# Kernel tuning notes

Measured on AMD Instinct MI355X. Metric: run time of the kernel, lower is better.

Reference implementation:

```python
import jax, jax.numpy as jnp
from jax import lax
import numpy as np

NLAYERS = 3
NHID = 256
NINP = 128
K = 2          # nstride (conv kernel size)
B = 32
W = 512


def _lstm_conv_layer(x_list, hid, ctx, conv_ws, conv_bs, rw, rb, aw):
    """One LSTM_conv(nl=len(conv_ws)) forward.
    x_list: list of [B, H, W]; hid: [nl+1, B, H, K]; ctx: [nl, B, H, K].
    Returns hx_all [B,H,W], cx_all [B,H,W], attn [B,W-1].
    """
    nl = len(conv_ws)
    ig = None
    for j in range(nl):
        # left-pad with last K-1 hidden columns, 'VALID' conv of kernel K -> length W
        padded = jnp.concatenate([hid[j][:, :, 1:], x_list[j]], axis=2)  # [B,H,W+K-1]
        y = lax.conv_general_dilated(padded, conv_ws[j], (1,), 'VALID',
                                     dimension_numbers=('NCH', 'OIH', 'NCH'))
        y = y + conv_bs[j][None, :, None]
        ig = y if ig is None else ig + y          # [B, 4H, W]

    hx0 = hid[nl][:, :, K - 1]                    # [B, H]
    cx0 = ctx[nl - 1][:, :, K - 1]                # [B, H]
    wsz = ig.shape[-1]
    ig_t = jnp.transpose(ig, (2, 0, 1))           # [W, B, 4H]
    not_last = jnp.arange(wsz) < (wsz - 1)

    def step(carry, inp):
        hx, cx = carry
        g_t, nl_flag = inp
        gates = g_t + hx @ rw.T + rb              # [B, 4H]
        i_g, f_g, c_g, o_g = jnp.split(gates, 4, axis=-1)  # torch fused LSTM order
        cx = jax.nn.sigmoid(f_g) * cx + jax.nn.sigmoid(i_g) * jnp.tanh(c_g)
        hx = jax.nn.sigmoid(o_g) * jnp.tanh(cx)
        a = jax.nn.sigmoid(hx @ aw)               # [B]
        hx = jnp.where(nl_flag, hx * a[:, None], hx)  # gate applied except at last step
        return (hx, cx), (hx, cx, a)

    _, (hs, cs, a_s) = lax.scan(step, (hx0, cx0), (ig_t, not_last))
    hx_all = jnp.transpose(hs, (1, 2, 0))         # [B, H, W]
    cx_all = jnp.transpose(cs, (1, 2, 0))
    attn = a_s[:-1].T                             # [B, W-1]
    return hx_all, cx_all, attn


def setup_inputs() -> dict:
    key = jax.random.key(0)
    ks = jax.random.split(key, 10)
    s = 0.02
    return {
        'input':   jax.random.normal(ks[0], (B, NINP, W), jnp.float32),
        'hidden':  jax.random.normal(ks[1], (NLAYERS + 1, B, NHID, K), jnp.float32),
        'context': jax.random.normal(ks[2], (NLAYERS, B, NHID, K), jnp.float32),
        'emb_w':   jax.random.normal(ks[3], (NHID, NINP), jnp.float32) * s,
        'emb_b':   jax.random.normal(ks[4], (NHID,), jnp.float32) * s,
        'conv_w':  jax.random.normal(ks[5], (6, 4 * NHID, NHID, K), jnp.float32) * s,
        'conv_b':  jax.random.normal(ks[6], (6, 4 * NHID), jnp.float32) * s,
        'rec_w':   jax.random.normal(ks[7], (NLAYERS, 4 * NHID, NHID), jnp.float32) * s,
        'rec_b':   jax.random.normal(ks[8], (NLAYERS, 4 * NHID), jnp.float32) * s,
        'attn_w':  jax.random.normal(ks[9], (NLAYERS, NHID), jnp.float32) * s,
    }


def reference(input, hidden, context, emb_w, emb_b, conv_w, conv_b, rec_w, rec_b, attn_w):
    # emb: Conv1d(ninp, nhid, 1)
    x0 = jnp.einsum('oc,bcw->bow', emb_w, input) + emb_b[None, :, None]  # [B,H,W]
    x_list = [x0]
    next_ctx = []
    attns = []
    off = 0
    for l in range(NLAYERS):
        nl = l + 1
        hx_all, cx_all, attn = _lstm_conv_layer(
            x_list, hidden[:nl + 1], context[:nl],
            [conv_w[off + j] for j in range(nl)],
            [conv_b[off + j] for j in range(nl)],
            rec_w[l], rec_b[l], attn_w[l])
        off += nl
        x_list.append(hx_all)
        next_ctx.append(cx_all)
        attns.append(attn)
    x = jnp.stack(x_list, 0)                      # [NLAYERS+1, B, H, W]
    nc = jnp.stack(next_ctx, 0)                   # [NLAYERS, B, H, W]
    attns = jnp.stack(attns, 0)                   # [NLAYERS, B, W-1]
    return x[:, :, :, -K:], nc[:, :, :, -K:], attns
```

## Files before the change

kernel.cpp:

```cpp
#include <hip/hip_runtime.h>


typedef _Float16 h2 __attribute__((ext_vector_type(2)));

static __device__ __forceinline__ float fdot2(unsigned a, unsigned b, float c) {
#if __has_builtin(__builtin_amdgcn_fdot2)
  return __builtin_amdgcn_fdot2(__builtin_bit_cast(h2, a),
                                __builtin_bit_cast(h2, b), c, false);
#else
  h2 x = __builtin_bit_cast(h2, a), y = __builtin_bit_cast(h2, b);
  return c + (float)x[0] * (float)y[0] + (float)x[1] * (float)y[1];
#endif
}

static __device__ __forceinline__ unsigned short f16b(float v) {
  _Float16 h = (_Float16)v;
  return __builtin_bit_cast(unsigned short, h);
}

static __device__ __forceinline__ float sigm(float x) {
  return 1.0f / (1.0f + __expf(-x));
}
static __device__ __forceinline__ float tanh_(float x) {
  return 1.0f - 2.0f / (1.0f + __expf(2.0f * x));
}

__global__ __launch_bounds__(256) void prep_rw(const float* __restrict__ rw,
                                               unsigned* __restrict__ rwp) {
  int idx = blockIdx.x * 256 + threadIdx.x;
  if (idx >= 3 * 131072) return;
  int l = idx / 131072, pos = idx % 131072;
  int tid, rl, j;
  if (pos < 98304) {
    int d = pos >> 9;
    tid = pos & 511;
    rl = d / 24;
    j = d % 24;
  } else {
    int p = pos - 98304;
    int c = p >> 11, rem = p & 2047;
    tid = rem >> 2;
    int k = rem & 3;
    rl = c >> 1;
    j = 24 + (c & 1) * 4 + k;
  }
  int s = tid & 3, u = tid >> 2;
  int row = (rl >> 1) * 256 + (rl & 1) * 128 + u;
  int cp = s * 32 + j;
  const float* src = rw + (l * 1024 + row) * 256 + 2 * cp;
  rwp[idx] = (unsigned)f16b(src[0]) | ((unsigned)f16b(src[1]) << 16);
}

__global__ __launch_bounds__(256) void prep_cw(const float* __restrict__ cw,
                                               unsigned* __restrict__ cwp) {
  int idx = blockIdx.x * 256 + threadIdx.x;
  if (idx >= 6 * 1024 * 2 * 128) return;
  int d = idx & 127, k = (idx >> 7) & 1, o = (idx >> 8) & 1023, jj = idx >> 18;
  const float* src = cw + ((jj * 1024 + o) * 256 + 2 * d) * 2 + k;
  unsigned v = (unsigned)f16b(src[0]) | ((unsigned)f16b(src[2]) << 16);
  cwp[idx] = v;
}

__global__ __launch_bounds__(256) void emb_kernel(
    const float* __restrict__ inp, const float* __restrict__ ew,
    const float* __restrict__ eb, unsigned short* __restrict__ x0f,
    float* __restrict__ out) {
  __shared__ float xt[32][65];
  __shared__ float wt[64][33];
  int b = blockIdx.z, w0 = blockIdx.x * 64, h0 = blockIdx.y * 64;
  int tid = threadIdx.x, tx = tid & 15, ty = tid >> 4;
  float acc[4][4] = {};
  for (int c0 = 0; c0 < 128; c0 += 32) {
    __syncthreads();
#pragma unroll
    for (int i = 0; i < 8; i++) {
      int f = i * 256 + tid, c = f >> 6, wl = f & 63;
      xt[c][wl] = inp[(b * 128 + c0 + c) * 512 + w0 + wl];
    }
#pragma unroll
    for (int i = 0; i < 8; i++) {
      int f = i * 256 + tid, h = f >> 5, c = f & 31;
      wt[h][c] = ew[(h0 + h) * 128 + c0 + c];
    }
    __syncthreads();
#pragma unroll
    for (int c = 0; c < 32; c++) {
      float xv[4], wv[4];
#pragma unroll
      for (int q = 0; q < 4; q++) xv[q] = xt[c][ty * 4 + q];
#pragma unroll
      for (int p = 0; p < 4; p++) wv[p] = wt[tx * 4 + p][c];
#pragma unroll
      for (int q = 0; q < 4; q++)
#pragma unroll
        for (int p = 0; p < 4; p++) acc[q][p] += xv[q] * wv[p];
    }
  }
#pragma unroll
  for (int q = 0; q < 4; q++) {
    int w = w0 + ty * 4 + q;
#pragma unroll
    for (int p = 0; p < 4; p++) {
      int h = h0 + tx * 4 + p;
      float v = acc[q][p] + eb[h];
      x0f[(b * 512 + w) * 256 + h] = f16b(v);
      if (w >= 510) out[(b * 256 + h) * 2 + (w - 510)] = v;
    }
  }
}

__global__ __launch_bounds__(256) void conv_kernel(
    const unsigned short* __restrict__ xf, const unsigned* __restrict__ cwp,
    const float* __restrict__ cb, const float* __restrict__ hidden,
    unsigned short* __restrict__ igf, int l, int off) {
  __shared__ __align__(16) unsigned xs[65][20];
  __shared__ __align__(16) unsigned wsm[2][16][66];
  int b = blockIdx.z, w0 = blockIdx.x * 64, o0 = blockIdx.y * 64;
  int tid = threadIdx.x, tx = tid & 15, ty = tid >> 4;
  float acc[4][4] = {};
  int nl = l + 1;
  for (int j = 0; j < nl; j++) {
    const unsigned* xj = (const unsigned*)(xf + j * 4194304 + b * 512 * 256);
    const unsigned* cwj = cwp + (off + j) * 262144;
    for (int c0 = 0; c0 < 256; c0 += 32) {
      int d0 = c0 >> 1;
      __syncthreads();
#pragma unroll
      for (int i = 0; i < 5; i++) {
        int f = i * 256 + tid;
        if (f < 1040) {
          int col = f >> 4, dw = f & 15;
          int w = w0 - 1 + col;
          unsigned v;
          if (w >= 0) {
            v = xj[w * 128 + d0 + dw];
          } else {
            const float* hp = hidden + ((j * 32 + b) * 256 + 2 * (d0 + dw)) * 2 + 1;
            v = (unsigned)f16b(hp[0]) | ((unsigned)f16b(hp[2]) << 16);
          }
          xs[col][dw] = v;
        }
      }
#pragma unroll
      for (int i = 0; i < 8; i++) {
        int f = i * 256 + tid;
        int oo = f >> 5, k = (f >> 4) & 1, dw = f & 15;
        wsm[k][dw][oo] = cwj[(o0 + oo) * 256 + k * 128 + d0 + dw];
      }
      __syncthreads();
#pragma unroll
      for (int g = 0; g < 4; g++) {
        uint4 xv[5];
#pragma unroll
        for (int q = 0; q < 5; q++)
          xv[q] = *(const uint4*)&xs[ty * 4 + q][g * 4];
#pragma unroll
        for (int p = 0; p < 4; p++) {
          unsigned wv0[4], wv1[4];
#pragma unroll
          for (int r = 0; r < 4; r++) {
            wv0[r] = wsm[0][g * 4 + r][tx * 4 + p];
            wv1[r] = wsm[1][g * 4 + r][tx * 4 + p];
          }
#pragma unroll
          for (int q = 0; q < 4; q++) {
            float a = acc[q][p];
            a = fdot2(wv0[0], xv[q].x, a);
            a = fdot2(wv0[1], xv[q].y, a);
            a = fdot2(wv0[2], xv[q].z, a);
            a = fdot2(wv0[3], xv[q].w, a);
            a = fdot2(wv1[0], xv[q + 1].x, a);
            a = fdot2(wv1[1], xv[q + 1].y, a);
            a = fdot2(wv1[2], xv[q + 1].z, a);
            a = fdot2(wv1[3], xv[q + 1].w, a);
            acc[q][p] = a;
          }
        }
      }
    }
  }
#pragma unroll
  for (int p = 0; p < 4; p++) {
    int o = o0 + tx * 4 + p;
    float bias = 0.f;
    for (int j = 0; j < nl; j++) bias += cb[(off + j) * 1024 + o];
#pragma unroll
    for (int q = 0; q < 4; q++) {
      int w = w0 + ty * 4 + q;
      igf[(b * 512 + w) * 1024 + o] = f16b(acc[q][p] + bias);
    }
  }
}

__global__ __launch_bounds__(512)
__attribute__((amdgpu_waves_per_eu(2, 2)))
void rec_kernel(const _Float16* __restrict__ igf, const unsigned* __restrict__ rwp_l,
                const float* __restrict__ rb, const float* __restrict__ aw,
                const float* __restrict__ hidden, const float* __restrict__ context,
                int l, unsigned short* __restrict__ xnext, float* __restrict__ out) {
  __shared__ __align__(16) uint4 w_lds4[16 * 512];
  __shared__ __align__(16) unsigned short hx_buf[2][256];
  __shared__ float red[2][8];
  int b = blockIdx.x, tid = threadIdx.x;
  int s = tid & 3, u = tid >> 2, lane = tid & 63, wid = tid >> 6;
  int hh = s & 1;
  int u2 = u + 128 * hh;

  unsigned wv[192];
#pragma unroll
  for (int d = 0; d < 192; d++) wv[d] = rwp_l[d * 512 + tid];
#pragma unroll
  for (int d = 0; d < 192; d++) asm volatile("" : "+v"(wv[d]));

  {
    const uint4* g16 = (const uint4*)(rwp_l + 98304);
#pragma unroll
    for (int c = 0; c < 16; c++) w_lds4[c * 512 + tid] = g16[c * 512 + tid];
  }

  float rb0 = rb[u2], rb1 = rb[256 + u2], rb2 = rb[512 + u2], rb3 = rb[768 + u2];
  float awj = aw[u2];
  float cx = context[((l * 32 + b) * 256 + u2) * 2 + 1];
  if (tid < 256)
    hx_buf[1][tid] = f16b(hidden[(((l + 1) * 32 + b) * 256 + tid) * 2 + 1]);
  float h_prev = 0.f;
  __syncthreads();

  const _Float16* igb = igf + (b * 512) * 1024 + u2;

  for (int t = 0; t < 512; t++) {
    int cur = t & 1, prv = cur ^ 1;
    const _Float16* ip = igb + t * 1024;
    float ig0 = (float)ip[0], ig1 = (float)ip[256];
    float ig2 = (float)ip[512], ig3 = (float)ip[768];
    float m_ = 1.0f;
    if (t) {
      const float* rp = red[prv];
      m_ = sigm(((rp[0] + rp[1]) + (rp[2] + rp[3])) +
                ((rp[4] + rp[5]) + (rp[6] + rp[7])));
    }

    float acc[8] = {};
    const uint4* hq = ((const uint4*)hx_buf[prv]) + 8 * s;
#pragma unroll
    for (int q = 0; q < 6; q++) {
      uint4 h = hq[q];
#pragma unroll
      for (int rl = 0; rl < 8; rl++) {
        acc[rl] = fdot2(wv[rl * 24 + q * 4 + 0], h.x, acc[rl]);
        acc[rl] = fdot2(wv[rl * 24 + q * 4 + 1], h.y, acc[rl]);
        acc[rl] = fdot2(wv[rl * 24 + q * 4 + 2], h.z, acc[rl]);
        acc[rl] = fdot2(wv[rl * 24 + q * 4 + 3], h.w, acc[rl]);
      }
    }
#pragma unroll
    for (int q = 6; q < 8; q++) {
      uint4 h = hq[q];
#pragma unroll
      for (int rl = 0; rl < 8; rl++) {
        uint4 lw = w_lds4[(rl * 2 + (q - 6)) * 512 + tid];
        acc[rl] = fdot2(lw.x, h.x, acc[rl]);
        acc[rl] = fdot2(lw.y, h.y, acc[rl]);
        acc[rl] = fdot2(lw.z, h.z, acc[rl]);
        acc[rl] = fdot2(lw.w, h.w, acc[rl]);
      }
    }
#pragma unroll
    for (int rl = 0; rl < 8; rl++) acc[rl] += __shfl_xor(acc[rl], 1);
#pragma unroll
    for (int rl = 0; rl < 8; rl++) acc[rl] += __shfl_xor(acc[rl], 2);

    float di = hh ? acc[1] : acc[0];
    float df = hh ? acc[3] : acc[2];
    float dc = hh ? acc[5] : acc[4];
    float do_ = hh ? acc[7] : acc[6];
    float g_i = ig0 + rb0 + m_ * di;
    float g_f = ig1 + rb1 + m_ * df;
    float g_c = ig2 + rb2 + m_ * dc;
    float g_o = ig3 + rb3 + m_ * do_;
    cx = sigm(g_f) * cx + sigm(g_i) * tanh_(g_c);
    float h_raw = sigm(g_o) * tanh_(cx);

    float part = (s < 2) ? h_raw * awj : 0.f;
#pragma unroll
    for (int sh = 32; sh > 0; sh >>= 1) part += __shfl_xor(part, sh);
    if (lane == 0) red[cur][wid] = part;

    if (s < 2) {
      hx_buf[cur][u2] = f16b(h_raw);
      if (t) {
        float hg = h_prev * m_;
        xnext[(b * 512 + (t - 1)) * 256 + u2] = f16b(hg);
        if (t == 511)
          out[(((l + 1) * 32 + b) * 256 + u2) * 2 + 0] = hg;
      }
      if (t >= 510)
        out[65536 + ((l * 32 + b) * 256 + u2) * 2 + (t - 510)] = cx;
    }
    if (tid == 0 && t) out[114688 + (l * 32 + b) * 511 + (t - 1)] = m_;
    h_prev = h_raw;
    __syncthreads();
  }
  if (s < 2) {
    xnext[(b * 512 + 511) * 256 + u2] = f16b(h_prev);
    out[(((l + 1) * 32 + b) * 256 + u2) * 2 + 1] = h_prev;
  }
}

extern "C" void kernel_launch(void* const* d_in, const int* in_sizes, int n_in,
                              void* d_out, int out_size, void* d_ws,
                              size_t ws_size, hipStream_t stream) {
  const float* input  = (const float*)d_in[0];
  const float* hidden = (const float*)d_in[1];
  const float* context= (const float*)d_in[2];
  const float* emb_w  = (const float*)d_in[3];
  const float* emb_b  = (const float*)d_in[4];
  const float* conv_w = (const float*)d_in[5];
  const float* conv_b = (const float*)d_in[6];
  const float* rec_w  = (const float*)d_in[7];
  const float* rec_b  = (const float*)d_in[8];
  const float* attn_w = (const float*)d_in[9];
  float* out = (float*)d_out;

  char* ws = (char*)d_ws;
  unsigned short* xf16 = (unsigned short*)ws;
  _Float16* igf = (_Float16*)(ws + 33554432);
  unsigned* rwp = (unsigned*)(ws + 67108864);
  unsigned* cwp = (unsigned*)(ws + 68681728);

  hipLaunchKernelGGL(prep_rw, dim3(1536), dim3(256), 0, stream, rec_w, rwp);
  hipLaunchKernelGGL(prep_cw, dim3(6144), dim3(256), 0, stream, conv_w, cwp);
  hipLaunchKernelGGL(emb_kernel, dim3(8, 4, 32), dim3(256), 0, stream,
                     input, emb_w, emb_b, xf16, out);
  int off = 0;
  for (int l = 0; l < 3; l++) {
    hipLaunchKernelGGL(conv_kernel, dim3(8, 16, 32), dim3(256), 0, stream,
                       xf16, cwp, conv_b, hidden, (unsigned short*)igf, l, off);
    hipLaunchKernelGGL(rec_kernel, dim3(32), dim3(512), 0, stream,
                       igf, rwp + l * 131072, rec_b + l * 1024,
                       attn_w + l * 256, hidden, context, l,
                       xf16 + (l + 1) * 4194304, out);
    off += l + 1;
  }
}
```

Measured before the change: 4.427 ms.

## Process two batch rows per recurrent block to reuse register-resident weights

The recurrent kernel now handles two batch elements per block (16 blocks instead of 32). Each weight fetched from registers or LDS is applied to both hidden vectors, and the threads that previously idled in the gate phase (s>=2) now compute the second batch's gates. To make room for the doubled accumulators, fewer weight words stay in registers (184 instead of 192) and more go to LDS, with the prep layout changed to match. The cost is twice the FMA work per block on each serial timestep, and only half the CUs are occupied.

```diff
diff --git a/kernel.cpp b/kernel.cpp
--- a/kernel.cpp
+++ b/kernel.cpp
@@ -31,18 +31,30 @@
   if (idx >= 3 * 131072) return;
   int l = idx / 131072, pos = idx % 131072;
   int tid, rl, j;
-  if (pos < 98304) {
+  if (pos < 94208) {
     int d = pos >> 9;
     tid = pos & 511;
-    rl = d / 24;
-    j = d % 24;
+    if (d < 40) {
+      rl = d / 20;
+      j = d % 20;
+    } else {
+      int e = d - 40;
+      rl = 2 + e / 24;
+      j = e % 24;
+    }
   } else {
-    int p = pos - 98304;
+    int p = pos - 94208;
     int c = p >> 11, rem = p & 2047;
     tid = rem >> 2;
-    int k = rem & 3;
-    rl = c >> 1;
-    j = 24 + (c & 1) * 4 + k;
+    int k = rem & 3, qL;
+    if (c < 6) {
+      rl = c / 3;
+      qL = 5 + c % 3;
+    } else {
+      rl = 2 + (c - 6) / 2;
+      qL = 6 + ((c - 6) & 1);
+    }
+    j = qL * 4 + k;
   }
   int s = tid & 3, u = tid >> 2;
   int row = (rl >> 1) * 256 + (rl & 1) * 128 + u;
@@ -198,31 +210,35 @@
                 const float* __restrict__ rb, const float* __restrict__ aw,
                 const float* __restrict__ hidden, const float* __restrict__ context,
                 int l, unsigned short* __restrict__ xnext, float* __restrict__ out) {
-  __shared__ __align__(16) uint4 w_lds4[16 * 512];
-  __shared__ __align__(16) unsigned short hx_buf[2][256];
-  __shared__ float red[2][8];
-  int b = blockIdx.x, tid = threadIdx.x;
+  __shared__ __align__(16) uint4 w_lds4[18 * 512];
+  __shared__ __align__(16) unsigned short hx_buf[2][2][256];
+  __shared__ float red[2][2][8];
+  int bp = blockIdx.x, tid = threadIdx.x;
   int s = tid & 3, u = tid >> 2, lane = tid & 63, wid = tid >> 6;
-  int hh = s & 1;
+  int hh = s & 1, bs = s >> 1;
   int u2 = u + 128 * hh;
-
-  unsigned wv[192];
-#pragma unroll
-  for (int d = 0; d < 192; d++) wv[d] = rwp_l[d * 512 + tid];
-#pragma unroll
-  for (int d = 0; d < 192; d++) asm volatile("" : "+v"(wv[d]));
+  int b = bp * 2 + bs;
+
+  unsigned wv[184];
+#pragma unroll
+  for (int d = 0; d < 184; d++) wv[d] = rwp_l[d * 512 + tid];
+#pragma unroll
+  for (int d = 0; d < 184; d++) asm volatile("" : "+v"(wv[d]));
 
   {
-    const uint4* g16 = (const uint4*)(rwp_l + 98304);
-#pragma unroll
-    for (int c = 0; c < 16; c++) w_lds4[c * 512 + tid] = g16[c * 512 + tid];
+    const uint4* g16 = (const uint4*)(rwp_l + 94208);
+#pragma unroll
+    for (int c = 0; c < 18; c++) w_lds4[c * 512 + tid] = g16[c * 512 + tid];
   }
 
   float rb0 = rb[u2], rb1 = rb[256 + u2], rb2 = rb[512 + u2], rb3 = rb[768 + u2];
   float awj = aw[u2];
   float cx = context[((l * 32 + b) * 256 + u2) * 2 + 1];
-  if (tid < 256)
-    hx_buf[1][tid] = f16b(hidden[(((l + 1) * 32 + b) * 256 + tid) * 2 + 1]);
+  {
+    int bb = tid >> 8, hu = tid & 255;
+    hx_buf[bb][1][hu] =
+        f16b(hidden[(((l + 1) * 32 + bp * 2 + bb) * 256 + hu) * 2 + 1]);
+  }
   float h_prev = 0.f;
   __syncthreads();
 
@@ -235,45 +251,93 @@
     float ig2 = (float)ip[512], ig3 = (float)ip[768];
     float m_ = 1.0f;
     if (t) {
-      const float* rp = red[prv];
+      const float* rp = red[bs][prv];
       m_ = sigm(((rp[0] + rp[1]) + (rp[2] + rp[3])) +
                 ((rp[4] + rp[5]) + (rp[6] + rp[7])));
     }
 
-    float acc[8] = {};
-    const uint4* hq = ((const uint4*)hx_buf[prv]) + 8 * s;
-#pragma unroll
-    for (int q = 0; q < 6; q++) {
-      uint4 h = hq[q];
+    float aA[8] = {}, aB[8] = {};
+    const uint4* hqA = ((const uint4*)hx_buf[0][prv]) + 8 * s;
+    const uint4* hqB = ((const uint4*)hx_buf[1][prv]) + 8 * s;
+#pragma unroll
+    for (int q = 0; q < 5; q++) {
+      uint4 hA = hqA[q], hB = hqB[q];
 #pragma unroll
       for (int rl = 0; rl < 8; rl++) {
-        acc[rl] = fdot2(wv[rl * 24 + q * 4 + 0], h.x, acc[rl]);
-        acc[rl] = fdot2(wv[rl * 24 + q * 4 + 1], h.y, acc[rl]);
-        acc[rl] = fdot2(wv[rl * 24 + q * 4 + 2], h.z, acc[rl]);
-        acc[rl] = fdot2(wv[rl * 24 + q * 4 + 3], h.w, acc[rl]);
-      }
-    }
-#pragma unroll
-    for (int q = 6; q < 8; q++) {
-      uint4 h = hq[q];
+        int base = (rl < 2) ? (rl * 20 + q * 4) : (40 + (rl - 2) * 24 + q * 4);
+        aA[rl] = fdot2(wv[base + 0], hA.x, aA[rl]);
+        aA[rl] = fdot2(wv[base + 1], hA.y, aA[rl]);
+        aA[rl] = fdot2(wv[base + 2], hA.z, aA[rl]);
+        aA[rl] = fdot2(wv[base + 3], hA.w, aA[rl]);
+        aB[rl] = fdot2(wv[base + 0], hB.x, aB[rl]);
+        aB[rl] = fdot2(wv[base + 1], hB.y, aB[rl]);
+        aB[rl] = fdot2(wv[base + 2], hB.z, aB[rl]);
+        aB[rl] = fdot2(wv[base + 3], hB.w, aB[rl]);
+      }
+    }
+    {
+      uint4 hA = hqA[5], hB = hqB[5];
+#pragma unroll
+      for (int rl = 0; rl < 2; rl++) {
+        uint4 lw = w_lds4[(rl * 3) * 512 + tid];
+        aA[rl] = fdot2(lw.x, hA.x, aA[rl]);
+        aA[rl] = fdot2(lw.y, hA.y, aA[rl]);
+        aA[rl] = fdot2(lw.z, hA.z, aA[rl]);
+        aA[rl] = fdot2(lw.w, hA.w, aA[rl]);
+        aB[rl] = fdot2(lw.x, hB.x, aB[rl]);
+        aB[rl] = fdot2(lw.y, hB.y, aB[rl]);
+        aB[rl] = fdot2(lw.z, hB.z, aB[rl]);
+        aB[rl] = fdot2(lw.w, hB.w, aB[rl]);
+      }
+#pragma unroll
+      for (int rl = 2; rl < 8; rl++) {
+        int base = 40 + (rl - 2) * 24 + 20;
+        aA[rl] = fdot2(wv[base + 0], hA.x, aA[rl]);
+        aA[rl] = fdot2(wv[base + 1], hA.y, aA[rl]);
+        aA[rl] = fdot2(wv[base + 2], hA.z, aA[rl]);
+        aA[rl] = fdot2(wv[base + 3], hA.w, aA[rl]);
+        aB[rl] = fdot2(wv[base + 0], hB.x, aB[rl]);
+        aB[rl] = fdot2(wv[base + 1], hB.y, aB[rl]);
+        aB[rl] = fdot2(wv[base + 2], hB.z, aB[rl]);
+        aB[rl] = fdot2(wv[base + 3], hB.w, aB[rl]);
+      }
+    }
+#pragma unroll
+    for (int qq = 6; qq < 8; qq++) {
+      uint4 hA = hqA[qq], hB = hqB[qq];
 #pragma unroll
       for (int rl = 0; rl < 8; rl++) {
-        uint4 lw = w_lds4[(rl * 2 + (q - 6)) * 512 + tid];
-        acc[rl] = fdot2(lw.x, h.x, acc[rl]);
-        acc[rl] = fdot2(lw.y, h.y, acc[rl]);
-        acc[rl] = fdot2(lw.z, h.z, acc[rl]);
-        acc[rl] = fdot2(lw.w, h.w, acc[rl]);
-      }
-    }
-#pragma unroll
-    for (int rl = 0; rl < 8; rl++) acc[rl] += __shfl_xor(acc[rl], 1);
-#pragma unroll
-    for (int rl = 0; rl < 8; rl++) acc[rl] += __shfl_xor(acc[rl], 2);
-
-    float di = hh ? acc[1] : acc[0];
-    float df = hh ? acc[3] : acc[2];
-    float dc = hh ? acc[5] : acc[4];
-    float do_ = hh ? acc[7] : acc[6];
+        int c = (rl < 2) ? (rl * 3 + (qq - 5)) : (6 + (rl - 2) * 2 + (qq - 6));
+        uint4 lw = w_lds4[c * 512 + tid];
+        aA[rl] = fdot2(lw.x, hA.x, aA[rl]);
+        aA[rl] = fdot2(lw.y, hA.y, aA[rl]);
+        aA[rl] = fdot2(lw.z, hA.z, aA[rl]);
+        aA[rl] = fdot2(lw.w, hA.w, aA[rl]);
+        aB[rl] = fdot2(lw.x, hB.x, aB[rl]);
+        aB[rl] = fdot2(lw.y, hB.y, aB[rl]);
+        aB[rl] = fdot2(lw.z, hB.z, aB[rl]);
+        aB[rl] = fdot2(lw.w, hB.w, aB[rl]);
+      }
+    }
+#pragma unroll
+    for (int rl = 0; rl < 8; rl++) {
+      aA[rl] += __shfl_xor(aA[rl], 1);
+      aB[rl] += __shfl_xor(aB[rl], 1);
+    }
+#pragma unroll
+    for (int rl = 0; rl < 8; rl++) {
+      aA[rl] += __shfl_xor(aA[rl], 2);
+      aB[rl] += __shfl_xor(aB[rl], 2);
+    }
+
+    float d0 = bs ? aB[0] : aA[0], d1 = bs ? aB[1] : aA[1];
+    float d2 = bs ? aB[2] : aA[2], d3 = bs ? aB[3] : aA[3];
+    float d4 = bs ? aB[4] : aA[4], d5 = bs ? aB[5] : aA[5];
+    float d6 = bs ? aB[6] : aA[6], d7 = bs ? aB[7] : aA[7];
+    float di = hh ? d1 : d0;
+    float df = hh ? d3 : d2;
+    float dc = hh ? d5 : d4;
+    float do_ = hh ? d7 : d6;
     float g_i = ig0 + rb0 + m_ * di;
     float g_f = ig1 + rb1 + m_ * df;
     float g_c = ig2 + rb2 + m_ * dc;
@@ -281,30 +345,31 @@
     cx = sigm(g_f) * cx + sigm(g_i) * tanh_(g_c);
     float h_raw = sigm(g_o) * tanh_(cx);
 
-    float part = (s < 2) ? h_raw * awj : 0.f;
-#pragma unroll
-    for (int sh = 32; sh > 0; sh >>= 1) part += __shfl_xor(part, sh);
-    if (lane == 0) red[cur][wid] = part;
-
-    if (s < 2) {
-      hx_buf[cur][u2] = f16b(h_raw);
-      if (t) {
-        float hg = h_prev * m_;
-        xnext[(b * 512 + (t - 1)) * 256 + u2] = f16b(hg);
-        if (t == 511)
-          out[(((l + 1) * 32 + b) * 256 + u2) * 2 + 0] = hg;
-      }
-      if (t >= 510)
-        out[65536 + ((l * 32 + b) * 256 + u2) * 2 + (t - 510)] = cx;
-    }
-    if (tid == 0 && t) out[114688 + (l * 32 + b) * 511 + (t - 1)] = m_;
+    float part = h_raw * awj;
+    part += __shfl_xor(part, 4);
+    part += __shfl_xor(part, 8);
+    part += __shfl_xor(part, 16);
+    part += __shfl_xor(part, 32);
+    part += __shfl_xor(part, 1);
+    if (lane == 0) red[0][cur][wid] = part;
+    if (lane == 2) red[1][cur][wid] = part;
+
+    hx_buf[bs][cur][u2] = f16b(h_raw);
+    if (t) {
+      float hg = h_prev * m_;
+      xnext[(b * 512 + (t - 1)) * 256 + u2] = f16b(hg);
+      if (t == 511)
+        out[(((l + 1) * 32 + b) * 256 + u2) * 2 + 0] = hg;
+    }
+    if (t >= 510)
+      out[65536 + ((l * 32 + b) * 256 + u2) * 2 + (t - 510)] = cx;
+    if (t && u == 0 && hh == 0)
+      out[114688 + (l * 32 + b) * 511 + (t - 1)] = m_;
     h_prev = h_raw;
     __syncthreads();
   }
-  if (s < 2) {
-    xnext[(b * 512 + 511) * 256 + u2] = f16b(h_prev);
-    out[(((l + 1) * 32 + b) * 256 + u2) * 2 + 1] = h_prev;
-  }
+  xnext[(b * 512 + 511) * 256 + u2] = f16b(h_prev);
+  out[(((l + 1) * 32 + b) * 256 + u2) * 2 + 1] = h_prev;
 }
 
 extern "C" void kernel_launch(void* const* d_in, const int* in_sizes, int n_in,
@@ -336,7 +401,7 @@
   for (int l = 0; l < 3; l++) {
     hipLaunchKernelGGL(conv_kernel, dim3(8, 16, 32), dim3(256), 0, stream,
                        xf16, cwp, conv_b, hidden, (unsigned short*)igf, l, off);
-    hipLaunchKernelGGL(rec_kernel, dim3(32), dim3(512), 0, stream,
+    hipLaunchKernelGGL(rec_kernel, dim3(16), dim3(512), 0, stream,
                        igf, rwp + l * 131072, rec_b + l * 1024,
                        attn_w + l * 256, hidden, context, l,
                        xf16 + (l + 1) * 4194304, out);
```

Result: slower. 6.894 ms (+55.7%).

## Move LDS-resident recurrent weights into AGPRs and pad hidden-state buffer

Applied to the files above, without the earlier changes.

The last quarter of the packed recurrent weights, previously staged in a 128KB LDS array and re-read every timestep, is now held in 64 accumulator registers (AGPRs) per thread, pinned there with inline asm constraints. The hidden-state LDS buffer is padded to 72-element rows so the four sub-lane groups read from different bank offsets. This removes per-step LDS weight traffic and possible bank conflicts on the hidden vector. The cost is AGPR-to-VGPR moves before each fdot2 and higher register pressure, which could cause spills or extra moves.

```diff
diff --git a/kernel.cpp b/kernel.cpp
--- a/kernel.cpp
+++ b/kernel.cpp
@@ -198,13 +198,13 @@
                 const float* __restrict__ rb, const float* __restrict__ aw,
                 const float* __restrict__ hidden, const float* __restrict__ context,
                 int l, unsigned short* __restrict__ xnext, float* __restrict__ out) {
-  __shared__ __align__(16) uint4 w_lds4[16 * 512];
-  __shared__ __align__(16) unsigned short hx_buf[2][256];
+  __shared__ __align__(16) unsigned short hx_buf[2][288];
   __shared__ float red[2][8];
   int b = blockIdx.x, tid = threadIdx.x;
   int s = tid & 3, u = tid >> 2, lane = tid & 63, wid = tid >> 6;
   int hh = s & 1;
   int u2 = u + 128 * hh;
+  int hxi = (u2 >> 6) * 72 + (u2 & 63);
 
   unsigned wv[192];
 #pragma unroll
@@ -212,17 +212,27 @@
 #pragma unroll
   for (int d = 0; d < 192; d++) asm volatile("" : "+v"(wv[d]));
 
+  unsigned wa[64];
   {
     const uint4* g16 = (const uint4*)(rwp_l + 98304);
 #pragma unroll
-    for (int c = 0; c < 16; c++) w_lds4[c * 512 + tid] = g16[c * 512 + tid];
-  }
+    for (int c = 0; c < 16; c++) {
+      uint4 g = g16[c * 512 + tid];
+      wa[c * 4 + 0] = g.x;
+      wa[c * 4 + 1] = g.y;
+      wa[c * 4 + 2] = g.z;
+      wa[c * 4 + 3] = g.w;
+    }
+  }
+#pragma unroll
+  for (int d = 0; d < 64; d++) asm volatile("" : "+a"(wa[d]));
 
   float rb0 = rb[u2], rb1 = rb[256 + u2], rb2 = rb[512 + u2], rb3 = rb[768 + u2];
   float awj = aw[u2];
   float cx = context[((l * 32 + b) * 256 + u2) * 2 + 1];
   if (tid < 256)
-    hx_buf[1][tid] = f16b(hidden[(((l + 1) * 32 + b) * 256 + tid) * 2 + 1]);
+    hx_buf[1][(tid >> 6) * 72 + (tid & 63)] =
+        f16b(hidden[(((l + 1) * 32 + b) * 256 + tid) * 2 + 1]);
   float h_prev = 0.f;
   __syncthreads();
 
@@ -241,7 +251,7 @@
     }
 
     float acc[8] = {};
-    const uint4* hq = ((const uint4*)hx_buf[prv]) + 8 * s;
+    const uint4* hq = (const uint4*)(&hx_buf[prv][s * 72]);
 #pragma unroll
     for (int q = 0; q < 6; q++) {
       uint4 h = hq[q];
@@ -258,11 +268,11 @@
       uint4 h = hq[q];
 #pragma unroll
       for (int rl = 0; rl < 8; rl++) {
-        uint4 lw = w_lds4[(rl * 2 + (q - 6)) * 512 + tid];
-        acc[rl] = fdot2(lw.x, h.x, acc[rl]);
-        acc[rl] = fdot2(lw.y, h.y, acc[rl]);
-        acc[rl] = fdot2(lw.z, h.z, acc[rl]);
-        acc[rl] = fdot2(lw.w, h.w, acc[rl]);
+        int c = rl * 2 + (q - 6);
+        acc[rl] = fdot2(wa[c * 4 + 0], h.x, acc[rl]);
+        acc[rl] = fdot2(wa[c * 4 + 1], h.y, acc[rl]);
+        acc[rl] = fdot2(wa[c * 4 + 2], h.z, acc[rl]);
+        acc[rl] = fdot2(wa[c * 4 + 3], h.w, acc[rl]);
       }
     }
 #pragma unroll
@@ -287,7 +297,7 @@
     if (lane == 0) red[cur][wid] = part;
 
     if (s < 2) {
-      hx_buf[cur][u2] = f16b(h_raw);
+      hx_buf[cur][hxi] = f16b(h_raw);
       if (t) {
         float hg = h_prev * m_;
         xnext[(b * 512 + (t - 1)) * 256 + u2] = f16b(hg);
```

After: 12.30 ms. +177.9%, slower.
